# Optimization experiments

Hardware: AMD Instinct MI355X
Metric: run time of the kernel (lower is better)

## Reference

```python
import jax, jax.numpy as jnp
import numpy as np

D_MODEL = 1024
H = 16
D_K = D_MODEL // H


def setup_inputs() -> dict:
    key = jax.random.key(0)
    ks = jax.random.split(key, 12)
    b, nq, nk = 2, 2048, 2048
    inp = {
        "queries": jax.random.normal(ks[0], (b, nq, D_MODEL), jnp.float32),
        "keys": jax.random.normal(ks[1], (b, nk, D_MODEL), jnp.float32),
        "values": jax.random.normal(ks[2], (b, nk, D_MODEL), jnp.float32),
        "query_mask": jax.random.uniform(ks[3], (b, nq), jnp.float32),
        "key_mask": jax.random.uniform(ks[4], (b, nk), jnp.float32),
        "attention_mask": jax.random.randint(ks[5], (b, 1, nq, nk), 0, 2).astype(bool),
        "attention_weights": jax.random.uniform(ks[6], (b, 1, nq, nk), jnp.float32),
        # Linear params init: normal(std=0.001) weights, zero bias (per init_weights)
        "Wq": 0.001 * jax.random.normal(ks[7], (D_MODEL, D_MODEL), jnp.float32),
        "Wk": 0.001 * jax.random.normal(ks[8], (D_MODEL, D_MODEL), jnp.float32),
        "Wv": 0.001 * jax.random.normal(ks[9], (D_MODEL, D_MODEL), jnp.float32),
        "Wo": 0.001 * jax.random.normal(ks[10], (D_MODEL, D_MODEL), jnp.float32),
        "bq": jnp.zeros((D_MODEL,), jnp.float32),
        "bk": jnp.zeros((D_MODEL,), jnp.float32),
        "bv": jnp.zeros((D_MODEL,), jnp.float32),
        "bo": jnp.zeros((D_MODEL,), jnp.float32),
    }
    return inp


def reference(queries, keys, values, query_mask, key_mask, attention_mask,
              attention_weights, Wq, Wk, Wv, Wo, bq, bk, bv, bo):
    b, nq, _ = queries.shape
    nk = keys.shape[1]
    # projections (torch Linear: x @ W.T + b)
    q = (queries @ Wq.T + bq).reshape(b, nq, H, D_K).transpose(0, 2, 1, 3)  # bhqd
    k = (keys @ Wk.T + bk).reshape(b, nk, H, D_K).transpose(0, 2, 1, 3)    # bhkd
    v = (values @ Wv.T + bv).reshape(b, nk, H, D_K).transpose(0, 2, 1, 3)  # bhkd
    # multiplicative per-token masks
    q = q * query_mask[:, None, :, None]
    k = k * key_mask[:, None, :, None]
    v = v * key_mask[:, None, :, None]
    att = jnp.einsum('bhqd,bhkd->bhqk', q, k) / np.sqrt(D_K).astype(np.float32)
    att = att * attention_weights
    att = jnp.where(attention_mask, -jnp.inf, att)
    att_softmax = jax.nn.softmax(att, axis=-1)
    # dropout is identity in eval/reference mode
    out = jnp.einsum('bhqk,bhkd->bhqd', att_softmax, v)
    out = out.transpose(0, 2, 1, 3).reshape(b, nq, H * D_K)
    out_final = out @ Wo.T + bo
    return (out_final, att_softmax)
```

## Files before the change

kernel.cpp:

```cpp
#include <hip/hip_runtime.h>

#define B2 2
#define NQ 2048
#define NK 2048
#define DM 1024
#define NH 16
#define DK 64
#define KC 64

typedef unsigned short u16;
typedef __attribute__((ext_vector_type(8))) short bf16x8;
typedef __attribute__((ext_vector_type(4))) float f32x4;

__device__ __forceinline__ u16 f2bf(float f) {
  unsigned u = __float_as_uint(f);
  u += 0x7FFFu + ((u >> 16) & 1u);
  return (u16)(u >> 16);
}
__device__ __forceinline__ float bf2f(u16 u) {
  return __uint_as_float(((unsigned)u) << 16);
}
__device__ __forceinline__ bf16x8 ld8f(const float* __restrict__ p) {
  const float4 a = *(const float4*)p;
  const float4 b = *(const float4*)(p + 4);
  bf16x8 v;
  v[0] = (short)f2bf(a.x); v[1] = (short)f2bf(a.y);
  v[2] = (short)f2bf(a.z); v[3] = (short)f2bf(a.w);
  v[4] = (short)f2bf(b.x); v[5] = (short)f2bf(b.y);
  v[6] = (short)f2bf(b.z); v[7] = (short)f2bf(b.w);
  return v;
}

#if __has_builtin(__builtin_amdgcn_exp2f)
#define EXP2F(x) __builtin_amdgcn_exp2f(x)
#else
#define EXP2F(x) exp2f(x)
#endif

#define MFMA(a, b, c) __builtin_amdgcn_mfma_f32_16x16x32_bf16(a, b, c, 0, 0, 0)

#define EXPC 0.18033688011112043f

__global__ __launch_bounds__(256) void k_fw(
    const float* __restrict__ attw, const int* __restrict__ amask, u16* __restrict__ fw) {
  const int i = (blockIdx.x * 256 + threadIdx.x) * 8;
#pragma unroll
  for (int hh = 0; hh < 2; hh++) {
    const float4 w = *(const float4*)(attw + i + 4 * hh);
    const int4 m = *(const int4*)(amask + i + 4 * hh);
    ushort4 o;
    o.x = m.x ? 0x7FC0 : f2bf(w.x);
    o.y = m.y ? 0x7FC0 : f2bf(w.y);
    o.z = m.z ? 0x7FC0 : f2bf(w.z);
    o.w = m.w ? 0x7FC0 : f2bf(w.w);
    *(ushort4*)(fw + i + 4 * hh) = o;
  }
}

template <bool AF32, bool WF32>
__device__ __forceinline__ void gemm_core(
    const void* __restrict__ Ap, const void* __restrict__ Wp,
    int tm, int tn, u16* As, u16* Bs, f32x4 acc[4][4]) {
  const int tid = threadIdx.x;
  const int lane = tid & 63;
  const int wid = tid >> 6;
  const int wm = (wid >> 1) * 64, wn = (wid & 1) * 64;
  const int cc = lane & 15, gg = lane >> 4;
  const int srow = tid >> 2, scol = 8 * (tid & 3);
  const size_t ra0 = (size_t)(tm + srow) * DM + scol;
  const size_t ra1 = (size_t)(tm + 64 + srow) * DM + scol;
  const size_t rb0 = (size_t)(tn + srow) * DM + scol;
  const size_t rb1 = (size_t)(tn + 64 + srow) * DM + scol;
  const float* Af = (const float*)Ap; const u16* Ab = (const u16*)Ap;
  const float* Wf = (const float*)Wp; const u16* Wb = (const u16*)Wp;
  const f32x4 Z4 = {0.f, 0.f, 0.f, 0.f};
#pragma unroll
  for (int i = 0; i < 4; i++)
#pragma unroll
    for (int j = 0; j < 4; j++) acc[i][j] = Z4;

#define LD_A(off) (AF32 ? ld8f(Af + (off)) : *(const bf16x8*)(Ab + (off)))
#define LD_W(off) (WF32 ? ld8f(Wf + (off)) : *(const bf16x8*)(Wb + (off)))
  *(bf16x8*)&As[tid * 8]        = LD_A(ra0);
  *(bf16x8*)&As[2048 + tid * 8] = LD_A(ra1);
  *(bf16x8*)&Bs[tid * 8]        = LD_W(rb0);
  *(bf16x8*)&Bs[2048 + tid * 8] = LD_W(rb1);

  int buf = 0;
  for (int kk = 0; kk < DM; kk += 32) {
    __syncthreads();
    const int o = buf * 4096;
    bf16x8 af[4], bv[4];
#pragma unroll
    for (int i = 0; i < 4; i++) af[i] = *(const bf16x8*)&As[o + (wm + i * 16 + cc) * 32 + 8 * gg];
#pragma unroll
    for (int i = 0; i < 4; i++) bv[i] = *(const bf16x8*)&Bs[o + (wn + i * 16 + cc) * 32 + 8 * gg];
    if (kk + 32 < DM) {
      const int p = (buf ^ 1) * 4096;
      *(bf16x8*)&As[p + tid * 8]        = LD_A(ra0 + kk + 32);
      *(bf16x8*)&As[p + 2048 + tid * 8] = LD_A(ra1 + kk + 32);
      *(bf16x8*)&Bs[p + tid * 8]        = LD_W(rb0 + kk + 32);
      *(bf16x8*)&Bs[p + 2048 + tid * 8] = LD_W(rb1 + kk + 32);
    }
#pragma unroll
    for (int mi = 0; mi < 4; mi++)
#pragma unroll
      for (int ni = 0; ni < 4; ni++) acc[mi][ni] = MFMA(af[mi], bv[ni], acc[mi][ni]);
    buf ^= 1;
  }
#undef LD_A
#undef LD_W
}

__global__ __launch_bounds__(256) void k_proj(
    const float* __restrict__ xq, const float* __restrict__ xk, const float* __restrict__ xv,
    const float* __restrict__ wq, const float* __restrict__ wk, const float* __restrict__ wv,
    const float* __restrict__ bq, const float* __restrict__ bk, const float* __restrict__ bv,
    const float* __restrict__ qmask, const float* __restrict__ kmask,
    u16* __restrict__ q_ws, u16* __restrict__ k_ws, u16* __restrict__ vT_ws) {
  __shared__ u16 As[2 * 4096];
  __shared__ u16 Bs[2 * 4096];
  const int bid = blockIdx.x;
  const int swz = (bid & 7) * 96 + (bid >> 3);
  const int tm = (swz & 31) * 128;
  const int yz = swz >> 5;
  const int tn = (yz & 7) * 128;
  const int z = yz >> 3;
  const float* A = (z == 0) ? xq : (z == 1) ? xk : xv;
  const float* Wm = (z == 0) ? wq : (z == 1) ? wk : wv;
  const float* bias = (z == 0) ? bq : (z == 1) ? bk : bv;
  const float* rmask = (z == 0) ? qmask : kmask;
  f32x4 acc[4][4];
  gemm_core<true, true>(A, Wm, tm, tn, As, Bs, acc);

  const int lane = threadIdx.x & 63;
  const int wid = threadIdx.x >> 6;
  const int wm = (wid >> 1) * 64, wn = (wid & 1) * 64;
  const int cc = lane & 15, gg = lane >> 4;
  const int b = tm >> 11;
  const int tok0 = tm & 2047;
#pragma unroll
  for (int mi = 0; mi < 4; mi++) {
    const int rl = wm + mi * 16 + 4 * gg;
    float rm[4];
#pragma unroll
    for (int r = 0; r < 4; r++) rm[r] = rmask[b * NQ + tok0 + rl + r];
#pragma unroll
    for (int ni = 0; ni < 4; ni++) {
      const int col = tn + wn + ni * 16 + cc;
      const int h = col >> 6, d = col & 63;
      const float bs = bias[col];
      f32x4 a = acc[mi][ni];
      if (z <= 1) {
        u16* dst = ((z == 0) ? q_ws : k_ws) +
                   ((size_t)(b * NH + h) * NQ + tok0 + rl) * DK + d;
#pragma unroll
        for (int r = 0; r < 4; r++) dst[(size_t)r * DK] = f2bf((a[r] + bs) * rm[r]);
      } else {
        ushort4 pk;
        pk.x = f2bf((a[0] + bs) * rm[0]);
        pk.y = f2bf((a[1] + bs) * rm[1]);
        pk.z = f2bf((a[2] + bs) * rm[2]);
        pk.w = f2bf((a[3] + bs) * rm[3]);
        *(ushort4*)(vT_ws + ((size_t)(b * NH + h) * DK + d) * NK + tok0 + rl) = pk;
      }
    }
  }
}

__global__ __launch_bounds__(256) void k_attn(
    const u16* __restrict__ q_ws, const u16* __restrict__ k_ws, const u16* __restrict__ vT_ws,
    const u16* __restrict__ fw, float* __restrict__ att_out, u16* __restrict__ ctxb) {
  __shared__ u16 Ks[128][72];
  __shared__ u16 Ps[4][16][72];
  const int bh = blockIdx.y;
  const int b = bh >> 4, hh = bh & 15;
  const int qb = blockIdx.x * 64;
  const int tid = threadIdx.x, lane = tid & 63, wid = tid >> 6;
  const int cc = lane & 15, gg = lane >> 4;
  const int qr0 = qb + wid * 16;
  const u16* qp = q_ws + ((size_t)bh * NQ + qr0 + cc) * DK + 8 * gg;
  const bf16x8 aq0 = *(const bf16x8*)qp;
  const bf16x8 aq1 = *(const bf16x8*)(qp + 32);
  const u16* fwrow = fw + ((size_t)b * NQ + qr0 + cc) * NK;
  const f32x4 Z4 = {0.f, 0.f, 0.f, 0.f};
  const int sr = tid >> 3, sc = 8 * (tid & 7);

  float sum = 0.f;
  for (int kc = 0; kc < NK; kc += 128) {
#pragma unroll
    for (int i = 0; i < 4; i++)
      *(bf16x8*)&Ks[i * 32 + sr][sc] =
          *(const bf16x8*)(k_ws + ((size_t)bh * NK + kc + i * 32 + sr) * DK + sc);
    __syncthreads();
#pragma unroll
    for (int n = 0; n < 8; n++) {
      const bf16x8 k0 = *(const bf16x8*)&Ks[n * 16 + cc][8 * gg];
      const bf16x8 k1 = *(const bf16x8*)&Ks[n * 16 + cc][32 + 8 * gg];
      f32x4 acc = Z4;
      acc = MFMA(k0, aq0, acc);
      acc = MFMA(k1, aq1, acc);
      const int k0i = kc + n * 16 + 4 * gg;
      const ushort4 fv = *(const ushort4*)(fwrow + k0i);
      const float e0 = EXP2F(acc[0] * bf2f(fv.x) * EXPC);
      const float e1 = EXP2F(acc[1] * bf2f(fv.y) * EXPC);
      const float e2 = EXP2F(acc[2] * bf2f(fv.z) * EXPC);
      const float e3 = EXP2F(acc[3] * bf2f(fv.w) * EXPC);
      sum += (e0 == e0) ? e0 : 0.f;
      sum += (e1 == e1) ? e1 : 0.f;
      sum += (e2 == e2) ? e2 : 0.f;
      sum += (e3 == e3) ? e3 : 0.f;
    }
    __syncthreads();
  }
  sum += __shfl_xor(sum, 16);
  sum += __shfl_xor(sum, 32);
  const float rinv = (sum > 0.f) ? 1.0f / sum : 0.f;

  f32x4 o[4];
#pragma unroll
  for (int i = 0; i < 4; i++) o[i] = Z4;
  float* attrow = att_out + (size_t)bh * NQ * NK + (size_t)(qr0 + cc) * NK;

  for (int kc = 0; kc < NK; kc += KC) {
#pragma unroll
    for (int i = 0; i < 2; i++) {
      *(bf16x8*)&Ks[i * 32 + sr][sc] =
          *(const bf16x8*)(k_ws + ((size_t)bh * NK + kc + i * 32 + sr) * DK + sc);
      *(bf16x8*)&Ks[64 + i * 32 + sr][sc] =
          *(const bf16x8*)(vT_ws + ((size_t)bh * DK + i * 32 + sr) * NK + kc + sc);
    }
    __syncthreads();
#pragma unroll
    for (int n = 0; n < 4; n++) {
      const bf16x8 k0 = *(const bf16x8*)&Ks[n * 16 + cc][8 * gg];
      const bf16x8 k1 = *(const bf16x8*)&Ks[n * 16 + cc][32 + 8 * gg];
      f32x4 acc = Z4;
      acc = MFMA(k0, aq0, acc);
      acc = MFMA(k1, aq1, acc);
      const int k0i = kc + n * 16 + 4 * gg;
      const ushort4 fv = *(const ushort4*)(fwrow + k0i);
      const float e0 = EXP2F(acc[0] * bf2f(fv.x) * EXPC);
      const float e1 = EXP2F(acc[1] * bf2f(fv.y) * EXPC);
      const float e2 = EXP2F(acc[2] * bf2f(fv.z) * EXPC);
      const float e3 = EXP2F(acc[3] * bf2f(fv.w) * EXPC);
      f32x4 pv;
      pv.x = (e0 == e0) ? e0 * rinv : 0.f;
      pv.y = (e1 == e1) ? e1 * rinv : 0.f;
      pv.z = (e2 == e2) ? e2 * rinv : 0.f;
      pv.w = (e3 == e3) ? e3 * rinv : 0.f;
      __builtin_nontemporal_store(pv, (f32x4*)(attrow + k0i));
      ushort4 pk;
      pk.x = f2bf(pv.x); pk.y = f2bf(pv.y); pk.z = f2bf(pv.z); pk.w = f2bf(pv.w);
      *(ushort4*)&Ps[wid][cc][n * 16 + 4 * gg] = pk;
    }
    const bf16x8 pa0 = *(const bf16x8*)&Ps[wid][cc][8 * gg];
    const bf16x8 pa1 = *(const bf16x8*)&Ps[wid][cc][32 + 8 * gg];
#pragma unroll
    for (int nd = 0; nd < 4; nd++) {
      const bf16x8 vb0 = *(const bf16x8*)&Ks[64 + nd * 16 + cc][8 * gg];
      const bf16x8 vb1 = *(const bf16x8*)&Ks[64 + nd * 16 + cc][32 + 8 * gg];
      o[nd] = MFMA(pa0, vb0, o[nd]);
      o[nd] = MFMA(pa1, vb1, o[nd]);
    }
    __syncthreads();
  }
#pragma unroll
  for (int nd = 0; nd < 4; nd++)
#pragma unroll
    for (int r = 0; r < 4; r++)
      ctxb[((size_t)b * NQ + qr0 + 4 * gg + r) * DM + hh * 64 + nd * 16 + cc] = f2bf(o[nd][r]);
}

__global__ __launch_bounds__(256) void k_oproj(
    const u16* __restrict__ ctxb, const float* __restrict__ wo,
    const float* __restrict__ bo, float* __restrict__ outp) {
  __shared__ u16 As[2 * 4096];
  __shared__ u16 Bs[2 * 4096];
  const int bid = blockIdx.x;
  const int swz = ((bid & 7) << 5) + (bid >> 3);
  const int tm = (swz & 31) * 128;
  const int tn = (swz >> 5) * 128;
  f32x4 acc[4][4];
  gemm_core<false, true>(ctxb, wo, tm, tn, As, Bs, acc);
  const int lane = threadIdx.x & 63;
  const int wid = threadIdx.x >> 6;
  const int wm = (wid >> 1) * 64, wn = (wid & 1) * 64;
  const int cc = lane & 15, gg = lane >> 4;
#pragma unroll
  for (int mi = 0; mi < 4; mi++) {
    const int rl = tm + wm + mi * 16 + 4 * gg;
#pragma unroll
    for (int ni = 0; ni < 4; ni++) {
      const int col = tn + wn + ni * 16 + cc;
      const float bs = bo[col];
      f32x4 a = acc[mi][ni];
#pragma unroll
      for (int r = 0; r < 4; r++) outp[(size_t)(rl + r) * DM + col] = a[r] + bs;
    }
  }
}

extern "C" void kernel_launch(void* const* d_in, const int* in_sizes, int n_in,
                              void* d_out, int out_size, void* d_ws, size_t ws_size,
                              hipStream_t stream) {
  (void)in_sizes; (void)n_in; (void)out_size; (void)ws_size;
  const float* queries = (const float*)d_in[0];
  const float* keys    = (const float*)d_in[1];
  const float* values  = (const float*)d_in[2];
  const float* qmask   = (const float*)d_in[3];
  const float* kmask   = (const float*)d_in[4];
  const int*   amask   = (const int*)d_in[5];
  const float* attw    = (const float*)d_in[6];
  const float* Wq = (const float*)d_in[7];
  const float* Wk = (const float*)d_in[8];
  const float* Wv = (const float*)d_in[9];
  const float* Wo = (const float*)d_in[10];
  const float* bq = (const float*)d_in[11];
  const float* bk = (const float*)d_in[12];
  const float* bv = (const float*)d_in[13];
  const float* bo = (const float*)d_in[14];

  float* outf = (float*)d_out;
  float* att_out = outf + (size_t)4194304;

  char* p = (char*)d_ws;
  u16* q_ws  = (u16*)p; p += (size_t)4194304 * 2;
  u16* k_ws  = (u16*)p; p += (size_t)4194304 * 2;
  u16* vT_ws = (u16*)p; p += (size_t)4194304 * 2;
  u16* ctxb  = (u16*)p; p += (size_t)4194304 * 2;
  u16* fw    = (u16*)p; p += (size_t)8388608 * 2;

  k_fw<<<dim3(4096, 1, 1), 256, 0, stream>>>(attw, amask, fw);
  k_proj<<<dim3(768, 1, 1), 256, 0, stream>>>(queries, keys, values, Wq, Wk, Wv,
                                              bq, bk, bv, qmask, kmask,
                                              q_ws, k_ws, vT_ws);
  k_attn<<<dim3(32, 32, 1), 256, 0, stream>>>(q_ws, k_ws, vT_ws, fw, att_out, ctxb);
  k_oproj<<<dim3(256, 1, 1), 256, 0, stream>>>(ctxb, Wo, bo, outf);
}
```

Baseline: 345.1 us.

## Fuse mask/weight prep into projection launch and drop LDS staging in attention

The separate mask/weight conversion kernel is folded into the projection kernel as 1024 extra grid-stride blocks, so the conversion overlaps with the projection GEMMs and one launch is saved. In the attention kernel, K and V^T tiles are no longer staged through shared memory with __syncthreads; each wave reads its MFMA operands straight from global memory (through cache) instead. This removes the barriers and LDS traffic but adds redundant global loads across the four waves, and the extra blocks may compete with the GEMM blocks for CUs.

```diff
diff --git a/kernel.cpp b/kernel.cpp
--- a/kernel.cpp
+++ b/kernel.cpp
@@ -6,7 +6,6 @@
 #define DM 1024
 #define NH 16
 #define DK 64
-#define KC 64
 
 typedef unsigned short u16;
 typedef __attribute__((ext_vector_type(8))) short bf16x8;
@@ -40,22 +39,6 @@
 #define MFMA(a, b, c) __builtin_amdgcn_mfma_f32_16x16x32_bf16(a, b, c, 0, 0, 0)
 
 #define EXPC 0.18033688011112043f
-
-__global__ __launch_bounds__(256) void k_fw(
-    const float* __restrict__ attw, const int* __restrict__ amask, u16* __restrict__ fw) {
-  const int i = (blockIdx.x * 256 + threadIdx.x) * 8;
-#pragma unroll
-  for (int hh = 0; hh < 2; hh++) {
-    const float4 w = *(const float4*)(attw + i + 4 * hh);
-    const int4 m = *(const int4*)(amask + i + 4 * hh);
-    ushort4 o;
-    o.x = m.x ? 0x7FC0 : f2bf(w.x);
-    o.y = m.y ? 0x7FC0 : f2bf(w.y);
-    o.z = m.z ? 0x7FC0 : f2bf(w.z);
-    o.w = m.w ? 0x7FC0 : f2bf(w.w);
-    *(ushort4*)(fw + i + 4 * hh) = o;
-  }
-}
 
 template <bool AF32, bool WF32>
 __device__ __forceinline__ void gemm_core(
@@ -117,10 +100,28 @@
     const float* __restrict__ wq, const float* __restrict__ wk, const float* __restrict__ wv,
     const float* __restrict__ bq, const float* __restrict__ bk, const float* __restrict__ bv,
     const float* __restrict__ qmask, const float* __restrict__ kmask,
-    u16* __restrict__ q_ws, u16* __restrict__ k_ws, u16* __restrict__ vT_ws) {
+    u16* __restrict__ q_ws, u16* __restrict__ k_ws, u16* __restrict__ vT_ws,
+    const float* __restrict__ attw, const int* __restrict__ amask, u16* __restrict__ fwo) {
+  const int bid = blockIdx.x;
+  if (bid >= 768) {
+    for (int i = ((bid - 768) * 256 + threadIdx.x) * 8; i < NQ * NK * B2;
+         i += 1024 * 256 * 8) {
+#pragma unroll
+      for (int hh = 0; hh < 2; hh++) {
+        const float4 w = *(const float4*)(attw + i + 4 * hh);
+        const int4 m = *(const int4*)(amask + i + 4 * hh);
+        ushort4 o;
+        o.x = m.x ? 0x7FC0 : f2bf(w.x);
+        o.y = m.y ? 0x7FC0 : f2bf(w.y);
+        o.z = m.z ? 0x7FC0 : f2bf(w.z);
+        o.w = m.w ? 0x7FC0 : f2bf(w.w);
+        *(ushort4*)(fwo + i + 4 * hh) = o;
+      }
+    }
+    return;
+  }
   __shared__ u16 As[2 * 4096];
   __shared__ u16 Bs[2 * 4096];
-  const int bid = blockIdx.x;
   const int swz = (bid & 7) * 96 + (bid >> 3);
   const int tm = (swz & 31) * 128;
   const int yz = swz >> 5;
@@ -171,7 +172,6 @@
 __global__ __launch_bounds__(256) void k_attn(
     const u16* __restrict__ q_ws, const u16* __restrict__ k_ws, const u16* __restrict__ vT_ws,
     const u16* __restrict__ fw, float* __restrict__ att_out, u16* __restrict__ ctxb) {
-  __shared__ u16 Ks[128][72];
   __shared__ u16 Ps[4][16][72];
   const int bh = blockIdx.y;
   const int b = bh >> 4, hh = bh & 15;
@@ -182,36 +182,29 @@
   const u16* qp = q_ws + ((size_t)bh * NQ + qr0 + cc) * DK + 8 * gg;
   const bf16x8 aq0 = *(const bf16x8*)qp;
   const bf16x8 aq1 = *(const bf16x8*)(qp + 32);
+  const u16* kbase = k_ws + (size_t)bh * NK * DK;
+  const u16* vbase = vT_ws + (size_t)bh * DK * NK;
   const u16* fwrow = fw + ((size_t)b * NQ + qr0 + cc) * NK;
   const f32x4 Z4 = {0.f, 0.f, 0.f, 0.f};
-  const int sr = tid >> 3, sc = 8 * (tid & 7);
 
   float sum = 0.f;
-  for (int kc = 0; kc < NK; kc += 128) {
-#pragma unroll
-    for (int i = 0; i < 4; i++)
-      *(bf16x8*)&Ks[i * 32 + sr][sc] =
-          *(const bf16x8*)(k_ws + ((size_t)bh * NK + kc + i * 32 + sr) * DK + sc);
-    __syncthreads();
-#pragma unroll
-    for (int n = 0; n < 8; n++) {
-      const bf16x8 k0 = *(const bf16x8*)&Ks[n * 16 + cc][8 * gg];
-      const bf16x8 k1 = *(const bf16x8*)&Ks[n * 16 + cc][32 + 8 * gg];
-      f32x4 acc = Z4;
-      acc = MFMA(k0, aq0, acc);
-      acc = MFMA(k1, aq1, acc);
-      const int k0i = kc + n * 16 + 4 * gg;
-      const ushort4 fv = *(const ushort4*)(fwrow + k0i);
-      const float e0 = EXP2F(acc[0] * bf2f(fv.x) * EXPC);
-      const float e1 = EXP2F(acc[1] * bf2f(fv.y) * EXPC);
-      const float e2 = EXP2F(acc[2] * bf2f(fv.z) * EXPC);
-      const float e3 = EXP2F(acc[3] * bf2f(fv.w) * EXPC);
-      sum += (e0 == e0) ? e0 : 0.f;
-      sum += (e1 == e1) ? e1 : 0.f;
-      sum += (e2 == e2) ? e2 : 0.f;
-      sum += (e3 == e3) ? e3 : 0.f;
-    }
-    __syncthreads();
+#pragma unroll 4
+  for (int t = 0; t < NK / 16; ++t) {
+    const u16* kr = kbase + (size_t)(t * 16 + cc) * DK + 8 * gg;
+    const bf16x8 k0 = *(const bf16x8*)kr;
+    const bf16x8 k1 = *(const bf16x8*)(kr + 32);
+    f32x4 acc = Z4;
+    acc = MFMA(k0, aq0, acc);
+    acc = MFMA(k1, aq1, acc);
+    const ushort4 fv = *(const ushort4*)(fwrow + t * 16 + 4 * gg);
+    const float e0 = EXP2F(acc[0] * bf2f(fv.x) * EXPC);
+    const float e1 = EXP2F(acc[1] * bf2f(fv.y) * EXPC);
+    const float e2 = EXP2F(acc[2] * bf2f(fv.z) * EXPC);
+    const float e3 = EXP2F(acc[3] * bf2f(fv.w) * EXPC);
+    sum += (e0 == e0) ? e0 : 0.f;
+    sum += (e1 == e1) ? e1 : 0.f;
+    sum += (e2 == e2) ? e2 : 0.f;
+    sum += (e3 == e3) ? e3 : 0.f;
   }
   sum += __shfl_xor(sum, 16);
   sum += __shfl_xor(sum, 32);
@@ -222,19 +215,12 @@
   for (int i = 0; i < 4; i++) o[i] = Z4;
   float* attrow = att_out + (size_t)bh * NQ * NK + (size_t)(qr0 + cc) * NK;
 
-  for (int kc = 0; kc < NK; kc += KC) {
-#pragma unroll
-    for (int i = 0; i < 2; i++) {
-      *(bf16x8*)&Ks[i * 32 + sr][sc] =
-          *(const bf16x8*)(k_ws + ((size_t)bh * NK + kc + i * 32 + sr) * DK + sc);
-      *(bf16x8*)&Ks[64 + i * 32 + sr][sc] =
-          *(const bf16x8*)(vT_ws + ((size_t)bh * DK + i * 32 + sr) * NK + kc + sc);
-    }
-    __syncthreads();
+  for (int kc = 0; kc < NK; kc += 64) {
 #pragma unroll
     for (int n = 0; n < 4; n++) {
-      const bf16x8 k0 = *(const bf16x8*)&Ks[n * 16 + cc][8 * gg];
-      const bf16x8 k1 = *(const bf16x8*)&Ks[n * 16 + cc][32 + 8 * gg];
+      const u16* kr = kbase + (size_t)(kc + n * 16 + cc) * DK + 8 * gg;
+      const bf16x8 k0 = *(const bf16x8*)kr;
+      const bf16x8 k1 = *(const bf16x8*)(kr + 32);
       f32x4 acc = Z4;
       acc = MFMA(k0, aq0, acc);
       acc = MFMA(k1, aq1, acc);
@@ -258,12 +244,12 @@
     const bf16x8 pa1 = *(const bf16x8*)&Ps[wid][cc][32 + 8 * gg];
 #pragma unroll
     for (int nd = 0; nd < 4; nd++) {
-      const bf16x8 vb0 = *(const bf16x8*)&Ks[64 + nd * 16 + cc][8 * gg];
-      const bf16x8 vb1 = *(const bf16x8*)&Ks[64 + nd * 16 + cc][32 + 8 * gg];
+      const u16* vr = vbase + (size_t)(nd * 16 + cc) * NK + kc + 8 * gg;
+      const bf16x8 vb0 = *(const bf16x8*)vr;
+      const bf16x8 vb1 = *(const bf16x8*)(vr + 32);
       o[nd] = MFMA(pa0, vb0, o[nd]);
       o[nd] = MFMA(pa1, vb1, o[nd]);
     }
-    __syncthreads();
   }
 #pragma unroll
   for (int nd = 0; nd < 4; nd++)
@@ -331,10 +317,9 @@
   u16* ctxb  = (u16*)p; p += (size_t)4194304 * 2;
   u16* fw    = (u16*)p; p += (size_t)8388608 * 2;
 
-  k_fw<<<dim3(4096, 1, 1), 256, 0, stream>>>(attw, amask, fw);
-  k_proj<<<dim3(768, 1, 1), 256, 0, stream>>>(queries, keys, values, Wq, Wk, Wv,
-                                              bq, bk, bv, qmask, kmask,
-                                              q_ws, k_ws, vT_ws);
+  k_proj<<<dim3(1792, 1, 1), 256, 0, stream>>>(queries, keys, values, Wq, Wk, Wv,
+                                               bq, bk, bv, qmask, kmask,
+                                               q_ws, k_ws, vT_ws, attw, amask, fw);
   k_attn<<<dim3(32, 32, 1), 256, 0, stream>>>(q_ws, k_ws, vT_ws, fw, att_out, ctxb);
   k_oproj<<<dim3(256, 1, 1), 256, 0, stream>>>(ctxb, Wo, bo, outf);
 }
```

Result: slower. 585.3 us (+69.6%).
